# Performance work log

Measured on AMD Instinct MI355X. Metric: run time of the kernel, lower is better.

## Reference

```python
import jax, jax.numpy as jnp
import numpy as np

E = 262144      # number of edges / neighbors
F = 128         # scalar feature dim
N_RBF = 20      # radial basis functions
RC = 5.0        # cosine cutoff radius


def setup_inputs() -> dict:
    key = jax.random.key(0)
    ks = jax.random.split(key, 9)
    s = jax.random.normal(ks[0], (E, F), dtype=jnp.float32)
    r = jax.random.normal(ks[1], (E, 3), dtype=jnp.float32)   # displacement vectors, |r|~1.7 < RC
    v = jax.random.normal(ks[2], (E, 3, F), dtype=jnp.float32)
    # learned params (fan-in scaled)
    W1 = jax.random.normal(ks[3], (F, F), dtype=jnp.float32) / np.sqrt(F)
    b1 = jnp.zeros((F,), dtype=jnp.float32)
    W2 = jax.random.normal(ks[4], (F, 3 * F), dtype=jnp.float32) / np.sqrt(F)
    b2 = jnp.zeros((3 * F,), dtype=jnp.float32)
    Wr = jax.random.normal(ks[5], (N_RBF, 3 * F), dtype=jnp.float32) / np.sqrt(N_RBF)
    br = jnp.zeros((3 * F,), dtype=jnp.float32)
    return {"s": s, "r": r, "v": v, "W1": W1, "b1": b1, "W2": W2, "b2": b2, "Wr": Wr, "br": br}


def reference(s, r, v, W1, b1, W2, b2, Wr, br):
    # PaiNN message block: RBF/cutoff-gated projections, hadamard splits, sum over edges.
    d = jnp.linalg.norm(r, axis=-1, keepdims=True)                  # [E,1]
    n = jnp.arange(1, N_RBF + 1, dtype=s.dtype)                     # [20]
    rbf = jnp.sin(n * jnp.pi * d / RC) / d                          # [E,20] sinc radial basis
    fcut = 0.5 * (jnp.cos(jnp.pi * d / RC) + 1.0) * (d < RC)        # [E,1] cosine cutoff
    # filter-generating network on scalar features
    phi = jax.nn.silu(s @ W1 + b1) @ W2 + b2                        # [E,384]
    Wfilt = (rbf @ Wr + br) * fcut                                  # [E,384]
    split = Wfilt * phi                                             # [E,384] hadamard gate
    wv1 = split[:, :F]            # gates existing vector features
    ws = split[:, F:2 * F]        # scalar message
    wv2 = split[:, 2 * F:]        # gates unit direction vectors
    out_s = jnp.sum(ws, axis=0)                                     # [128]
    unit_r = r / d                                                  # [E,3]
    dv = unit_r[:, :, None] * wv2[:, None, :] + wv1[:, None, :] * v # [E,3,128]
    out_v = jnp.sum(dv, axis=0)                                     # [3,128]
    return (out_v, out_s)
```

## Files before the change

kernel.cpp:

```cpp
#include <hip/hip_runtime.h>


#define E_TOT  262144
#define NTILES 16384
#define NBLK   512
#define PART_STRIDE 896

typedef __attribute__((ext_vector_type(8))) short bf16x8;
typedef __attribute__((ext_vector_type(4))) float f32x4;
typedef __attribute__((ext_vector_type(4))) unsigned short u16x4;

static __device__ __forceinline__ unsigned short f2bf(float f) {
  union { float f; unsigned u; } x; x.f = f;
  unsigned r = x.u + 0x7fffu + ((x.u >> 16) & 1u);
  return (unsigned short)(r >> 16);
}
static __device__ __forceinline__ float bf2f(unsigned short h) {
  union { unsigned u; float f; } x; x.u = ((unsigned)h) << 16;
  return x.f;
}

#define BAR() do {                                           \
    asm volatile("s_waitcnt lgkmcnt(0)" ::: "memory");       \
    __builtin_amdgcn_s_barrier();                            \
    asm volatile("" ::: "memory");                           \
  } while (0)

__global__ void prep_kernel(const float* __restrict__ W1, const float* __restrict__ W2,
                            const float* __restrict__ Wr,
                            unsigned short* __restrict__ w1t, unsigned short* __restrict__ w2t,
                            unsigned short* __restrict__ wrt) {
  int idx = blockIdx.x * 256 + threadIdx.x;
  if (idx < 16384) {
    int k = idx >> 7, c = idx & 127;
    float x = W1[idx];
    unsigned short hi = f2bf(x);
    w1t[c * 128 + k] = hi;
    w1t[16384 + c * 128 + k] = f2bf(x - bf2f(hi));
  } else if (idx < 65536) {
    int i = idx - 16384;
    int k = i / 384, c = i % 384;
    float x = W2[i];
    unsigned short hi = f2bf(x);
    w2t[c * 128 + k] = hi;
    w2t[49152 + c * 128 + k] = f2bf(x - bf2f(hi));
  } else if (idx < 77824) {
    int i = idx - 65536;
    int c = i >> 5, n = i & 31;
    float x = (n < 20) ? Wr[n * 384 + c] : 0.0f;
    unsigned short hi = f2bf(x);
    wrt[c * 32 + n] = hi;
    wrt[12288 + c * 32 + n] = f2bf(x - bf2f(hi));
  }
}

__global__ __launch_bounds__(512, 2) void painn_main(
    const float* __restrict__ s, const float* __restrict__ r, const float* __restrict__ v,
    const float* __restrict__ b1, const float* __restrict__ b2, const float* __restrict__ br,
    const unsigned short* __restrict__ w1t, const unsigned short* __restrict__ w2t,
    const unsigned short* __restrict__ wrt, float* __restrict__ partials)
{
  __shared__ __align__(16) unsigned short sAh[16][136], sAl[16][136];
  __shared__ __align__(16) unsigned short hAh[16][136], hAl[16][136];
  __shared__ __align__(16) unsigned short rbfh[2][16][40], rbfl[2][16][40];
  __shared__ float4 urA[2][16];

  const int tid = threadIdx.x;
  const int wv  = tid >> 6;
  const int ln  = tid & 63;
  const int l15 = ln & 15;
  const int q4  = ln >> 4;
  const int jcol = wv * 16 + l15;

  for (int i = tid; i < 2 * 16 * 12; i += 512) {
    const int b = i / 192, rw = (i / 12) % 16, cc = 20 + (i % 12);
    rbfh[b][rw][cc] = 0; rbfl[b][rw][cc] = 0;
  }

  bf16x8 w1fh[4], w1fl[4];
#pragma unroll
  for (int ks = 0; ks < 4; ++ks) {
    w1fh[ks] = *(const bf16x8*)(w1t + jcol * 128 + ks * 32 + q4 * 8);
    w1fl[ks] = *(const bf16x8*)(w1t + 16384 + jcol * 128 + ks * 32 + q4 * 8);
  }
  const float b1v = b1[jcol];

  float b2v[3], brv[3];
  bf16x8 w2fh[3][4], w2fl[3][4], wrfh[3], wrfl[3];
#pragma unroll
  for (int fci = 0; fci < 3; ++fci) {
    const int j = jcol + fci * 128;
    b2v[fci] = b2[j];
    brv[fci] = br[j];
#pragma unroll
    for (int ks = 0; ks < 4; ++ks) {
      w2fh[fci][ks] = *(const bf16x8*)(w2t + j * 128 + ks * 32 + q4 * 8);
      w2fl[fci][ks] = *(const bf16x8*)(w2t + 49152 + j * 128 + ks * 32 + q4 * 8);
    }
    wrfh[fci] = *(const bf16x8*)(wrt + j * 32 + q4 * 8);
    wrfl[fci] = *(const bf16x8*)(wrt + 12288 + j * 32 + q4 * 8);
  }

  float accS = 0.f;
  float accV1[3] = {0.f, 0.f, 0.f};
  float accV2[3] = {0.f, 0.f, 0.f};
  const f32x4 zero4 = {0.f, 0.f, 0.f, 0.f};

  const int srow = tid >> 5;
  const int sc4  = (tid & 31) * 4;
  float4 pf = *(const float4*)(s + (size_t)((size_t)blockIdx.x * 16 + srow) * 128 + sc4);
  float rx = 0.f, ry = 0.f, rz = 0.f;
  if (tid < 320) {
    const float* rp = r + ((size_t)blockIdx.x * 16 + (tid & 15)) * 3;
    rx = rp[0]; ry = rp[1]; rz = rp[2];
  }

  int p = 0;
  for (int t = blockIdx.x; t < NTILES; t += NBLK, p ^= 1) {
    const int e0 = t * 16;

    float vp[4][3];
    {
      const float* vb = v + (size_t)e0 * 384 + jcol;
#pragma unroll
      for (int rr = 0; rr < 4; ++rr) {
        const int el = q4 * 4 + rr;
#pragma unroll
        for (int c = 0; c < 3; ++c)
          vp[rr][c] = vb[(size_t)el * 384 + c * 128];
      }
    }

    {
      u16x4 vh, vl;
      unsigned short h0 = f2bf(pf.x); vh[0] = h0; vl[0] = f2bf(pf.x - bf2f(h0));
      unsigned short h1 = f2bf(pf.y); vh[1] = h1; vl[1] = f2bf(pf.y - bf2f(h1));
      unsigned short h2 = f2bf(pf.z); vh[2] = h2; vl[2] = f2bf(pf.z - bf2f(h2));
      unsigned short h3 = f2bf(pf.w); vh[3] = h3; vl[3] = f2bf(pf.w - bf2f(h3));
      *(u16x4*)&sAh[srow][sc4] = vh;
      *(u16x4*)&sAl[srow][sc4] = vl;
    }
    if (tid < 320) {
      const float d = sqrtf(rx * rx + ry * ry + rz * rz);
      const float inv = 1.0f / d;
      const int n = tid >> 4;
      const float val = sinf(0.62831853071795864f * (float)(n + 1) * d) * inv;
      const unsigned short hi = f2bf(val);
      rbfh[p][tid & 15][n] = hi;
      rbfl[p][tid & 15][n] = f2bf(val - bf2f(hi));
      if (tid < 16) {
        const float fcut = (d < 5.0f) ? 0.5f * (cosf(0.62831853071795864f * d) + 1.0f) : 0.0f;
        float4 u4; u4.x = rx * inv; u4.y = ry * inv; u4.z = rz * inv; u4.w = fcut;
        urA[p][tid] = u4;
      }
    }
    BAR();

    f32x4 hacc = zero4;
#pragma unroll
    for (int ks = 0; ks < 4; ++ks) {
      const bf16x8 ah = *(const bf16x8*)&sAh[l15][ks * 32 + q4 * 8];
      const bf16x8 al = *(const bf16x8*)&sAl[l15][ks * 32 + q4 * 8];
      hacc = __builtin_amdgcn_mfma_f32_16x16x32_bf16(ah, w1fh[ks], hacc, 0, 0, 0);
      hacc = __builtin_amdgcn_mfma_f32_16x16x32_bf16(al, w1fh[ks], hacc, 0, 0, 0);
      hacc = __builtin_amdgcn_mfma_f32_16x16x32_bf16(ah, w1fl[ks], hacc, 0, 0, 0);
    }
#pragma unroll
    for (int rr = 0; rr < 4; ++rr) {
      const float x = hacc[rr] + b1v;
      const float hvv = x / (1.0f + __expf(-x));
      const unsigned short hi = f2bf(hvv);
      hAh[q4 * 4 + rr][jcol] = hi;
      hAl[q4 * 4 + rr][jcol] = f2bf(hvv - bf2f(hi));
    }

    {
      int tn = t + NBLK;
      if (tn >= NTILES) tn = blockIdx.x;
      pf = *(const float4*)(s + (size_t)((size_t)tn * 16 + srow) * 128 + sc4);
      if (tid < 320) {
        const float* rp = r + ((size_t)tn * 16 + (tid & 15)) * 3;
        rx = rp[0]; ry = rp[1]; rz = rp[2];
      }
    }
    BAR();

    f32x4 wacc[3], pacc[3];
    {
      const bf16x8 rh = *(const bf16x8*)&rbfh[p][l15][q4 * 8];
      const bf16x8 rl = *(const bf16x8*)&rbfl[p][l15][q4 * 8];
#pragma unroll
      for (int fci = 0; fci < 3; ++fci) {
        f32x4 a = __builtin_amdgcn_mfma_f32_16x16x32_bf16(rh, wrfh[fci], zero4, 0, 0, 0);
        a = __builtin_amdgcn_mfma_f32_16x16x32_bf16(rl, wrfh[fci], a, 0, 0, 0);
        a = __builtin_amdgcn_mfma_f32_16x16x32_bf16(rh, wrfl[fci], a, 0, 0, 0);
        wacc[fci] = a;
        pacc[fci] = zero4;
      }
    }
#pragma unroll
    for (int ks = 0; ks < 4; ++ks) {
      const bf16x8 ah = *(const bf16x8*)&hAh[l15][ks * 32 + q4 * 8];
      const bf16x8 al = *(const bf16x8*)&hAl[l15][ks * 32 + q4 * 8];
#pragma unroll
      for (int fci = 0; fci < 3; ++fci) {
        pacc[fci] = __builtin_amdgcn_mfma_f32_16x16x32_bf16(ah, w2fh[fci][ks], pacc[fci], 0, 0, 0);
        pacc[fci] = __builtin_amdgcn_mfma_f32_16x16x32_bf16(al, w2fh[fci][ks], pacc[fci], 0, 0, 0);
        pacc[fci] = __builtin_amdgcn_mfma_f32_16x16x32_bf16(ah, w2fl[fci][ks], pacc[fci], 0, 0, 0);
      }
    }

#pragma unroll
    for (int rr = 0; rr < 4; ++rr) {
      const float4 u4 = urA[p][q4 * 4 + rr];
      const float sp0 = u4.w * (wacc[0][rr] + brv[0]) * (pacc[0][rr] + b2v[0]);
      const float sp1 = u4.w * (wacc[1][rr] + brv[1]) * (pacc[1][rr] + b2v[1]);
      const float sp2 = u4.w * (wacc[2][rr] + brv[2]) * (pacc[2][rr] + b2v[2]);
      accV1[0] += sp0 * vp[rr][0];
      accV1[1] += sp0 * vp[rr][1];
      accV1[2] += sp0 * vp[rr][2];
      accS += sp1;
      accV2[0] += sp2 * u4.x;
      accV2[1] += sp2 * u4.y;
      accV2[2] += sp2 * u4.z;
    }
  }

  float* pb = partials + (size_t)blockIdx.x * PART_STRIDE;
#pragma unroll
  for (int c = 0; c < 3; ++c) {
    float tv = accV1[c];
    tv += __shfl_xor(tv, 16);
    tv += __shfl_xor(tv, 32);
    if (ln < 16) pb[c * 128 + jcol] = tv;
  }
  {
    float tv = accS;
    tv += __shfl_xor(tv, 16);
    tv += __shfl_xor(tv, 32);
    if (ln < 16) pb[768 + jcol] = tv;
  }
#pragma unroll
  for (int c = 0; c < 3; ++c) {
    float tv = accV2[c];
    tv += __shfl_xor(tv, 16);
    tv += __shfl_xor(tv, 32);
    if (ln < 16) pb[384 + c * 128 + jcol] = tv;
  }
}

__global__ void reduce_kernel(const float* __restrict__ partials, float* __restrict__ out) {
  const int o = blockIdx.x * 256 + threadIdx.x;
  float a0 = 0.f, a1 = 0.f, a2 = 0.f, a3 = 0.f;
  if (o < 384) {
#pragma unroll 4
    for (int b = 0; b < NBLK; b += 4) {
      a0 += partials[(size_t)(b + 0) * PART_STRIDE + o] + partials[(size_t)(b + 0) * PART_STRIDE + 384 + o];
      a1 += partials[(size_t)(b + 1) * PART_STRIDE + o] + partials[(size_t)(b + 1) * PART_STRIDE + 384 + o];
      a2 += partials[(size_t)(b + 2) * PART_STRIDE + o] + partials[(size_t)(b + 2) * PART_STRIDE + 384 + o];
      a3 += partials[(size_t)(b + 3) * PART_STRIDE + o] + partials[(size_t)(b + 3) * PART_STRIDE + 384 + o];
    }
    out[o] = (a0 + a1) + (a2 + a3);
  } else {
    const int j = o - 384;
#pragma unroll 4
    for (int b = 0; b < NBLK; b += 4) {
      a0 += partials[(size_t)(b + 0) * PART_STRIDE + 768 + j];
      a1 += partials[(size_t)(b + 1) * PART_STRIDE + 768 + j];
      a2 += partials[(size_t)(b + 2) * PART_STRIDE + 768 + j];
      a3 += partials[(size_t)(b + 3) * PART_STRIDE + 768 + j];
    }
    out[o] = (a0 + a1) + (a2 + a3);
  }
}

extern "C" void kernel_launch(void* const* d_in, const int* in_sizes, int n_in,
                              void* d_out, int out_size, void* d_ws, size_t ws_size,
                              hipStream_t stream) {
  const float* s  = (const float*)d_in[0];
  const float* r  = (const float*)d_in[1];
  const float* v  = (const float*)d_in[2];
  const float* W1 = (const float*)d_in[3];
  const float* b1 = (const float*)d_in[4];
  const float* W2 = (const float*)d_in[5];
  const float* b2 = (const float*)d_in[6];
  const float* Wr = (const float*)d_in[7];
  const float* br = (const float*)d_in[8];
  float* out = (float*)d_out;

  char* ws = (char*)d_ws;
  float* partials = (float*)ws;
  unsigned short* w1t = (unsigned short*)(ws + (size_t)NBLK * PART_STRIDE * 4);
  unsigned short* w2t = w1t + 32768;
  unsigned short* wrt = w2t + 98304;

  prep_kernel<<<304, 256, 0, stream>>>(W1, W2, Wr, w1t, w2t, wrt);
  painn_main<<<NBLK, 512, 0, stream>>>(s, r, v, b1, b2, br, w1t, w2t, wrt, partials);
  reduce_kernel<<<2, 256, 0, stream>>>(partials, out);
}
```

Baseline: 728.0 us.

## Process 32-edge tiles per iteration with two interleaved MFMA chains

```diff
diff --git a/kernel.cpp b/kernel.cpp
--- a/kernel.cpp
+++ b/kernel.cpp
@@ -2,13 +2,14 @@
 
 
 #define E_TOT  262144
-#define NTILES 16384
+#define NTILES 8192
 #define NBLK   512
 #define PART_STRIDE 896
 
 typedef __attribute__((ext_vector_type(8))) short bf16x8;
 typedef __attribute__((ext_vector_type(4))) float f32x4;
-typedef __attribute__((ext_vector_type(4))) unsigned short u16x4;
+
+union U8 { bf16x8 v; unsigned short u[8]; };
 
 static __device__ __forceinline__ unsigned short f2bf(float f) {
   union { float f; unsigned u; } x; x.f = f;
@@ -60,10 +61,10 @@
     const unsigned short* __restrict__ w1t, const unsigned short* __restrict__ w2t,
     const unsigned short* __restrict__ wrt, float* __restrict__ partials)
 {
-  __shared__ __align__(16) unsigned short sAh[16][136], sAl[16][136];
-  __shared__ __align__(16) unsigned short hAh[16][136], hAl[16][136];
-  __shared__ __align__(16) unsigned short rbfh[2][16][40], rbfl[2][16][40];
-  __shared__ float4 urA[2][16];
+  __shared__ __align__(16) unsigned short sAh[32][136], sAl[32][136];
+  __shared__ __align__(16) unsigned short hAh[32][136], hAl[32][136];
+  __shared__ __align__(16) unsigned short rbfh[2][32][40], rbfl[2][32][40];
+  __shared__ float4 urA[2][32];
 
   const int tid = threadIdx.x;
   const int wv  = tid >> 6;
@@ -72,8 +73,8 @@
   const int q4  = ln >> 4;
   const int jcol = wv * 16 + l15;
 
-  for (int i = tid; i < 2 * 16 * 12; i += 512) {
-    const int b = i / 192, rw = (i / 12) % 16, cc = 20 + (i % 12);
+  for (int i = tid; i < 2 * 32 * 12; i += 512) {
+    const int b = i / 384, rw = (i / 12) % 32, cc = 20 + (i % 12);
     rbfh[b][rw][cc] = 0; rbfl[b][rw][cc] = 0;
   }
 
@@ -106,49 +107,68 @@
   float accV2[3] = {0.f, 0.f, 0.f};
   const f32x4 zero4 = {0.f, 0.f, 0.f, 0.f};
 
-  const int srow = tid >> 5;
-  const int sc4  = (tid & 31) * 4;
-  float4 pf = *(const float4*)(s + (size_t)((size_t)blockIdx.x * 16 + srow) * 128 + sc4);
-  float rx = 0.f, ry = 0.f, rz = 0.f;
-  if (tid < 320) {
-    const float* rp = r + ((size_t)blockIdx.x * 16 + (tid & 15)) * 3;
+  const int srow = tid >> 4;
+  const int sc8  = (tid & 15) * 8;
+  float4 pfa, pfb;
+  {
+    const float* sp = s + (size_t)((size_t)blockIdx.x * 32 + srow) * 128 + sc8;
+    pfa = *(const float4*)sp;
+    pfb = *(const float4*)(sp + 4);
+  }
+  float rx, ry, rz;
+  {
+    const float* rp = r + ((size_t)blockIdx.x * 32 + (tid & 31)) * 3;
     rx = rp[0]; ry = rp[1]; rz = rp[2];
   }
 
   int p = 0;
   for (int t = blockIdx.x; t < NTILES; t += NBLK, p ^= 1) {
-    const int e0 = t * 16;
-
-    float vp[4][3];
+    const int e0 = t * 32;
+
+    float vp0[4][3], vp1[4][3];
     {
       const float* vb = v + (size_t)e0 * 384 + jcol;
 #pragma unroll
       for (int rr = 0; rr < 4; ++rr) {
-        const int el = q4 * 4 + rr;
-#pragma unroll
-        for (int c = 0; c < 3; ++c)
-          vp[rr][c] = vb[(size_t)el * 384 + c * 128];
-      }
-    }
-
-    {
-      u16x4 vh, vl;
-      unsigned short h0 = f2bf(pf.x); vh[0] = h0; vl[0] = f2bf(pf.x - bf2f(h0));
-      unsigned short h1 = f2bf(pf.y); vh[1] = h1; vl[1] = f2bf(pf.y - bf2f(h1));
-      unsigned short h2 = f2bf(pf.z); vh[2] = h2; vl[2] = f2bf(pf.z - bf2f(h2));
-      unsigned short h3 = f2bf(pf.w); vh[3] = h3; vl[3] = f2bf(pf.w - bf2f(h3));
-      *(u16x4*)&sAh[srow][sc4] = vh;
-      *(u16x4*)&sAl[srow][sc4] = vl;
-    }
-    if (tid < 320) {
+        const int el0 = q4 * 4 + rr;
+#pragma unroll
+        for (int c = 0; c < 3; ++c) {
+          vp0[rr][c] = vb[(size_t)el0 * 384 + c * 128];
+          vp1[rr][c] = vb[(size_t)(16 + el0) * 384 + c * 128];
+        }
+      }
+    }
+
+    {
+      U8 vh, vl;
+      unsigned short h0 = f2bf(pfa.x); vh.u[0] = h0; vl.u[0] = f2bf(pfa.x - bf2f(h0));
+      unsigned short h1 = f2bf(pfa.y); vh.u[1] = h1; vl.u[1] = f2bf(pfa.y - bf2f(h1));
+      unsigned short h2 = f2bf(pfa.z); vh.u[2] = h2; vl.u[2] = f2bf(pfa.z - bf2f(h2));
+      unsigned short h3 = f2bf(pfa.w); vh.u[3] = h3; vl.u[3] = f2bf(pfa.w - bf2f(h3));
+      unsigned short h4 = f2bf(pfb.x); vh.u[4] = h4; vl.u[4] = f2bf(pfb.x - bf2f(h4));
+      unsigned short h5 = f2bf(pfb.y); vh.u[5] = h5; vl.u[5] = f2bf(pfb.y - bf2f(h5));
+      unsigned short h6 = f2bf(pfb.z); vh.u[6] = h6; vl.u[6] = f2bf(pfb.z - bf2f(h6));
+      unsigned short h7 = f2bf(pfb.w); vh.u[7] = h7; vl.u[7] = f2bf(pfb.w - bf2f(h7));
+      *(bf16x8*)&sAh[srow][sc8] = vh.v;
+      *(bf16x8*)&sAl[srow][sc8] = vl.v;
+    }
+    {
       const float d = sqrtf(rx * rx + ry * ry + rz * rz);
       const float inv = 1.0f / d;
-      const int n = tid >> 4;
+      const int e_ = tid & 31;
+      const int n  = tid >> 5;
       const float val = sinf(0.62831853071795864f * (float)(n + 1) * d) * inv;
       const unsigned short hi = f2bf(val);
-      rbfh[p][tid & 15][n] = hi;
-      rbfl[p][tid & 15][n] = f2bf(val - bf2f(hi));
-      if (tid < 16) {
+      rbfh[p][e_][n] = hi;
+      rbfl[p][e_][n] = f2bf(val - bf2f(hi));
+      if (tid < 128) {
+        const int n2 = 16 + n;
+        const float v2 = sinf(0.62831853071795864f * (float)(n2 + 1) * d) * inv;
+        const unsigned short hi2 = f2bf(v2);
+        rbfh[p][e_][n2] = hi2;
+        rbfl[p][e_][n2] = f2bf(v2 - bf2f(hi2));
+      }
+      if (tid < 32) {
         const float fcut = (d < 5.0f) ? 0.5f * (cosf(0.62831853071795864f * d) + 1.0f) : 0.0f;
         float4 u4; u4.x = rx * inv; u4.y = ry * inv; u4.z = rz * inv; u4.w = fcut;
         urA[p][tid] = u4;
@@ -156,73 +176,112 @@
     }
     BAR();
 
-    f32x4 hacc = zero4;
+    f32x4 hacc0 = zero4, hacc1 = zero4;
 #pragma unroll
     for (int ks = 0; ks < 4; ++ks) {
-      const bf16x8 ah = *(const bf16x8*)&sAh[l15][ks * 32 + q4 * 8];
-      const bf16x8 al = *(const bf16x8*)&sAl[l15][ks * 32 + q4 * 8];
-      hacc = __builtin_amdgcn_mfma_f32_16x16x32_bf16(ah, w1fh[ks], hacc, 0, 0, 0);
-      hacc = __builtin_amdgcn_mfma_f32_16x16x32_bf16(al, w1fh[ks], hacc, 0, 0, 0);
-      hacc = __builtin_amdgcn_mfma_f32_16x16x32_bf16(ah, w1fl[ks], hacc, 0, 0, 0);
+      const bf16x8 a0h = *(const bf16x8*)&sAh[l15][ks * 32 + q4 * 8];
+      const bf16x8 a0l = *(const bf16x8*)&sAl[l15][ks * 32 + q4 * 8];
+      const bf16x8 a1h = *(const bf16x8*)&sAh[16 + l15][ks * 32 + q4 * 8];
+      const bf16x8 a1l = *(const bf16x8*)&sAl[16 + l15][ks * 32 + q4 * 8];
+      hacc0 = __builtin_amdgcn_mfma_f32_16x16x32_bf16(a0h, w1fh[ks], hacc0, 0, 0, 0);
+      hacc1 = __builtin_amdgcn_mfma_f32_16x16x32_bf16(a1h, w1fh[ks], hacc1, 0, 0, 0);
+      hacc0 = __builtin_amdgcn_mfma_f32_16x16x32_bf16(a0l, w1fh[ks], hacc0, 0, 0, 0);
+      hacc1 = __builtin_amdgcn_mfma_f32_16x16x32_bf16(a1l, w1fh[ks], hacc1, 0, 0, 0);
+      hacc0 = __builtin_amdgcn_mfma_f32_16x16x32_bf16(a0h, w1fl[ks], hacc0, 0, 0, 0);
+      hacc1 = __builtin_amdgcn_mfma_f32_16x16x32_bf16(a1h, w1fl[ks], hacc1, 0, 0, 0);
     }
 #pragma unroll
     for (int rr = 0; rr < 4; ++rr) {
-      const float x = hacc[rr] + b1v;
-      const float hvv = x / (1.0f + __expf(-x));
-      const unsigned short hi = f2bf(hvv);
-      hAh[q4 * 4 + rr][jcol] = hi;
-      hAl[q4 * 4 + rr][jcol] = f2bf(hvv - bf2f(hi));
+      {
+        const float x = hacc0[rr] + b1v;
+        const float hvv = x / (1.0f + __expf(-x));
+        const unsigned short hi = f2bf(hvv);
+        hAh[q4 * 4 + rr][jcol] = hi;
+        hAl[q4 * 4 + rr][jcol] = f2bf(hvv - bf2f(hi));
+      }
+      {
+        const float x = hacc1[rr] + b1v;
+        const float hvv = x / (1.0f + __expf(-x));
+        const unsigned short hi = f2bf(hvv);
+        hAh[16 + q4 * 4 + rr][jcol] = hi;
+        hAl[16 + q4 * 4 + rr][jcol] = f2bf(hvv - bf2f(hi));
+      }
     }
 
     {
       int tn = t + NBLK;
       if (tn >= NTILES) tn = blockIdx.x;
-      pf = *(const float4*)(s + (size_t)((size_t)tn * 16 + srow) * 128 + sc4);
-      if (tid < 320) {
-        const float* rp = r + ((size_t)tn * 16 + (tid & 15)) * 3;
-        rx = rp[0]; ry = rp[1]; rz = rp[2];
-      }
+      const float* sp = s + (size_t)((size_t)tn * 32 + srow) * 128 + sc8;
+      pfa = *(const float4*)sp;
+      pfb = *(const float4*)(sp + 4);
+      const float* rp = r + ((size_t)tn * 32 + (tid & 31)) * 3;
+      rx = rp[0]; ry = rp[1]; rz = rp[2];
     }
     BAR();
 
-    f32x4 wacc[3], pacc[3];
-    {
-      const bf16x8 rh = *(const bf16x8*)&rbfh[p][l15][q4 * 8];
-      const bf16x8 rl = *(const bf16x8*)&rbfl[p][l15][q4 * 8];
+    f32x4 wacc0[3], wacc1[3], pacc0[3], pacc1[3];
+    {
+      const bf16x8 r0h = *(const bf16x8*)&rbfh[p][l15][q4 * 8];
+      const bf16x8 r0l = *(const bf16x8*)&rbfl[p][l15][q4 * 8];
+      const bf16x8 r1h = *(const bf16x8*)&rbfh[p][16 + l15][q4 * 8];
+      const bf16x8 r1l = *(const bf16x8*)&rbfl[p][16 + l15][q4 * 8];
 #pragma unroll
       for (int fci = 0; fci < 3; ++fci) {
-        f32x4 a = __builtin_amdgcn_mfma_f32_16x16x32_bf16(rh, wrfh[fci], zero4, 0, 0, 0);
-        a = __builtin_amdgcn_mfma_f32_16x16x32_bf16(rl, wrfh[fci], a, 0, 0, 0);
-        a = __builtin_amdgcn_mfma_f32_16x16x32_bf16(rh, wrfl[fci], a, 0, 0, 0);
-        wacc[fci] = a;
-        pacc[fci] = zero4;
+        f32x4 a0 = __builtin_amdgcn_mfma_f32_16x16x32_bf16(r0h, wrfh[fci], zero4, 0, 0, 0);
+        f32x4 a1 = __builtin_amdgcn_mfma_f32_16x16x32_bf16(r1h, wrfh[fci], zero4, 0, 0, 0);
+        a0 = __builtin_amdgcn_mfma_f32_16x16x32_bf16(r0l, wrfh[fci], a0, 0, 0, 0);
+        a1 = __builtin_amdgcn_mfma_f32_16x16x32_bf16(r1l, wrfh[fci], a1, 0, 0, 0);
+        a0 = __builtin_amdgcn_mfma_f32_16x16x32_bf16(r0h, wrfl[fci], a0, 0, 0, 0);
+        a1 = __builtin_amdgcn_mfma_f32_16x16x32_bf16(r1h, wrfl[fci], a1, 0, 0, 0);
+        wacc0[fci] = a0; wacc1[fci] = a1;
+        pacc0[fci] = zero4; pacc1[fci] = zero4;
       }
     }
 #pragma unroll
     for (int ks = 0; ks < 4; ++ks) {
-      const bf16x8 ah = *(const bf16x8*)&hAh[l15][ks * 32 + q4 * 8];
-      const bf16x8 al = *(const bf16x8*)&hAl[l15][ks * 32 + q4 * 8];
+      const bf16x8 a0h = *(const bf16x8*)&hAh[l15][ks * 32 + q4 * 8];
+      const bf16x8 a0l = *(const bf16x8*)&hAl[l15][ks * 32 + q4 * 8];
+      const bf16x8 a1h = *(const bf16x8*)&hAh[16 + l15][ks * 32 + q4 * 8];
+      const bf16x8 a1l = *(const bf16x8*)&hAl[16 + l15][ks * 32 + q4 * 8];
 #pragma unroll
       for (int fci = 0; fci < 3; ++fci) {
-        pacc[fci] = __builtin_amdgcn_mfma_f32_16x16x32_bf16(ah, w2fh[fci][ks], pacc[fci], 0, 0, 0);
-        pacc[fci] = __builtin_amdgcn_mfma_f32_16x16x32_bf16(al, w2fh[fci][ks], pacc[fci], 0, 0, 0);
-        pacc[fci] = __builtin_amdgcn_mfma_f32_16x16x32_bf16(ah, w2fl[fci][ks], pacc[fci], 0, 0, 0);
+        pacc0[fci] = __builtin_amdgcn_mfma_f32_16x16x32_bf16(a0h, w2fh[fci][ks], pacc0[fci], 0, 0, 0);
+        pacc1[fci] = __builtin_amdgcn_mfma_f32_16x16x32_bf16(a1h, w2fh[fci][ks], pacc1[fci], 0, 0, 0);
+        pacc0[fci] = __builtin_amdgcn_mfma_f32_16x16x32_bf16(a0l, w2fh[fci][ks], pacc0[fci], 0, 0, 0);
+        pacc1[fci] = __builtin_amdgcn_mfma_f32_16x16x32_bf16(a1l, w2fh[fci][ks], pacc1[fci], 0, 0, 0);
+        pacc0[fci] = __builtin_amdgcn_mfma_f32_16x16x32_bf16(a0h, w2fl[fci][ks], pacc0[fci], 0, 0, 0);
+        pacc1[fci] = __builtin_amdgcn_mfma_f32_16x16x32_bf16(a1h, w2fl[fci][ks], pacc1[fci], 0, 0, 0);
       }
     }
 
 #pragma unroll
     for (int rr = 0; rr < 4; ++rr) {
-      const float4 u4 = urA[p][q4 * 4 + rr];
-      const float sp0 = u4.w * (wacc[0][rr] + brv[0]) * (pacc[0][rr] + b2v[0]);
-      const float sp1 = u4.w * (wacc[1][rr] + brv[1]) * (pacc[1][rr] + b2v[1]);
-      const float sp2 = u4.w * (wacc[2][rr] + brv[2]) * (pacc[2][rr] + b2v[2]);
-      accV1[0] += sp0 * vp[rr][0];
-      accV1[1] += sp0 * vp[rr][1];
-      accV1[2] += sp0 * vp[rr][2];
-      accS += sp1;
-      accV2[0] += sp2 * u4.x;
-      accV2[1] += sp2 * u4.y;
-      accV2[2] += sp2 * u4.z;
+      {
+        const float4 u4 = urA[p][q4 * 4 + rr];
+        const float sp0 = u4.w * (wacc0[0][rr] + brv[0]) * (pacc0[0][rr] + b2v[0]);
+        const float sp1 = u4.w * (wacc0[1][rr] + brv[1]) * (pacc0[1][rr] + b2v[1]);
+        const float sp2 = u4.w * (wacc0[2][rr] + brv[2]) * (pacc0[2][rr] + b2v[2]);
+        accV1[0] += sp0 * vp0[rr][0];
+        accV1[1] += sp0 * vp0[rr][1];
+        accV1[2] += sp0 * vp0[rr][2];
+        accS += sp1;
+        accV2[0] += sp2 * u4.x;
+        accV2[1] += sp2 * u4.y;
+        accV2[2] += sp2 * u4.z;
+      }
+      {
+        const float4 u4 = urA[p][16 + q4 * 4 + rr];
+        const float sp0 = u4.w * (wacc1[0][rr] + brv[0]) * (pacc1[0][rr] + b2v[0]);
+        const float sp1 = u4.w * (wacc1[1][rr] + brv[1]) * (pacc1[1][rr] + b2v[1]);
+        const float sp2 = u4.w * (wacc1[2][rr] + brv[2]) * (pacc1[2][rr] + b2v[2]);
+        accV1[0] += sp0 * vp1[rr][0];
+        accV1[1] += sp0 * vp1[rr][1];
+        accV1[2] += sp0 * vp1[rr][2];
+        accS += sp1;
+        accV2[0] += sp2 * u4.x;
+        accV2[1] += sp2 * u4.y;
+        accV2[2] += sp2 * u4.z;
+      }
     }
   }
 
```

Result: slower. 854.5 us (+17.4%).
